# Performance work log

Measured on AMD Instinct MI355X. Metric: run time of the kernel, lower is better.

The kernel has to match this reference:

```python
import jax, jax.numpy as jnp
import numpy as np

G = 5      # kan_grid: number of grid intervals on [-1, 1]
K = 3      # kan_k: B-spline order

def make_grid(in_dim, dtype=jnp.float32):
    # pykan extended grid: uniform on [-1,1] with G intervals, extended by K knots each side
    h = 2.0 / G
    pts = jnp.arange(-K, G + K + 1, dtype=dtype) * h - 1.0   # (G + 2K + 1,)
    return jnp.broadcast_to(pts, (in_dim, G + 2 * K + 1))

def b_spline_basis(x, grid):
    # x: (N, D), grid: (D, M).  Cox-de Boor recursion, vectorized over (N, D).
    xe = x[:, :, None]                      # (N, D, 1)
    g = grid[None, :, :]                    # (1, D, M)
    B = ((xe >= g[:, :, :-1]) & (xe < g[:, :, 1:])).astype(x.dtype)  # order 0
    for p in range(1, K + 1):
        B = ((xe - g[:, :, :-(p + 1)]) / (g[:, :, p:-1] - g[:, :, :-(p + 1)])) * B[:, :, :-1] \
          + ((g[:, :, p + 1:] - xe) / (g[:, :, p + 1:] - g[:, :, 1:-p])) * B[:, :, 1:]
    return B                                # (N, D, G + K)

def kan_layer(x, coef, scale_base, scale_sp):
    # pykan KANLayer: out_o = sum_i [ sb[i,o]*silu(x_i) + ss[i,o]*sum_g B(x_i)_g * coef[i,o,g] ]
    in_dim = x.shape[1]
    B = b_spline_basis(x, make_grid(in_dim, x.dtype))          # (N, D, G+K)
    y_base = jnp.einsum('ni,io->no', jax.nn.silu(x), scale_base)
    y_sp = jnp.einsum('nig,iog,io->no', B, coef, scale_sp)
    return y_base + y_sp

def setup_inputs() -> dict:
    key = jax.random.key(0)
    ks = jax.random.split(key, 5)
    d_model, hidden = 512, 1024
    bsz, seq = 4, 1024
    ncoef = G + K
    x = jax.random.normal(ks[0], (bsz, seq, d_model), dtype=jnp.float32)
    coef1 = 0.1 * jax.random.normal(ks[1], (d_model, hidden, ncoef), dtype=jnp.float32)
    coef2 = 0.1 * jax.random.normal(ks[2], (hidden, d_model, ncoef), dtype=jnp.float32)
    scale_base1 = (1.0 / np.sqrt(d_model)) * jax.random.normal(ks[3], (d_model, hidden), dtype=jnp.float32)
    scale_base2 = (1.0 / np.sqrt(hidden)) * jax.random.normal(ks[4], (hidden, d_model), dtype=jnp.float32)
    scale_sp1 = jnp.ones((d_model, hidden), dtype=jnp.float32)
    scale_sp2 = jnp.ones((hidden, d_model), dtype=jnp.float32)
    return {"x": x, "coef1": coef1, "scale_base1": scale_base1, "scale_sp1": scale_sp1,
            "coef2": coef2, "scale_base2": scale_base2, "scale_sp2": scale_sp2}

def reference(x, coef1, scale_base1, scale_sp1, coef2, scale_base2, scale_sp2):
    bsz, seq, d_model = x.shape
    flat = x.reshape(-1, d_model)                      # (N, d_model); chunking is math-neutral
    h = kan_layer(flat, coef1, scale_base1, scale_sp1)  # (N, hidden)
    out = kan_layer(h, coef2, scale_base2, scale_sp2)   # (N, d_model)
    return out.reshape(bsz, seq, d_model)              # dropout p=0.0 -> identity
```

## Files before the change

kernel.cpp:

```cpp
#include <hip/hip_runtime.h>
#include <hip/hip_bf16.h>
#include <cstdint>
#include <cstddef>

typedef float  f32x4 __attribute__((ext_vector_type(4)));
typedef _Float16 f16x8 __attribute__((ext_vector_type(8)));

#define DEVFN __device__ __forceinline__

DEVFN void bspline8(float x, float bv[8]) {
    float t[12];
#pragma unroll
    for (int j = 0; j < 12; ++j) t[j] = (float)(j - 3) * 0.4f - 1.0f;
    float B[11];
#pragma unroll
    for (int j = 0; j < 11; ++j) B[j] = (x >= t[j] && x < t[j + 1]) ? 1.0f : 0.0f;
    const float rp[3] = {2.5f, 1.25f, 0.8333333333f};
#pragma unroll
    for (int p = 1; p <= 3; ++p) {
#pragma unroll
        for (int j = 0; j + p < 11; ++j) {
            float left  = (x - t[j]) * rp[p - 1];
            float right = (t[j + p + 1] - x) * rp[p - 1];
            B[j] = left * B[j] + right * B[j + 1];
        }
    }
#pragma unroll
    for (int g = 0; g < 8; ++g) bv[g] = B[g];
}

DEVFN void kan_features(float x, _Float16* dst, int D) {
    float s = x * __builtin_amdgcn_rcpf(1.0f + __expf(-x));
    float bv[8];
    bspline8(x, bv);
    dst[0] = (_Float16)s;
#pragma unroll
    for (int g = 0; g < 8; ++g) dst[(size_t)(g + 1) * D] = (_Float16)bv[g];
}

__global__ void prep_a_kernel(const float* __restrict__ X,
                              _Float16* __restrict__ Aaug,
                              int total, int dshift) {
    int idx = blockIdx.x * 256 + threadIdx.x;
    if (idx >= total) return;
    const int D = 1 << dshift;
    const int K = 9 << dshift;
    const int n = idx >> dshift;
    const int i = idx & (D - 1);
    kan_features(X[idx], Aaug + (size_t)n * K + i, D);
}

__global__ void prep_a_red_kernel(const float* __restrict__ HP,
                                  _Float16* __restrict__ Aaug,
                                  int total, int dshift, size_t pstride) {
    int idx = blockIdx.x * 256 + threadIdx.x;
    if (idx >= total) return;
    const int D = 1 << dshift;
    const int K = 9 << dshift;
    const int n = idx >> dshift;
    const int i = idx & (D - 1);
    float x = (HP[idx] + HP[idx + pstride]) +
              (HP[idx + 2 * pstride] + HP[idx + 3 * pstride]);
    kan_features(x, Aaug + (size_t)n * K + i, D);
}

__global__ void reduce_out_kernel(const float* __restrict__ OP,
                                  float* __restrict__ out,
                                  int total4, size_t pstride4) {
    int i = blockIdx.x * 256 + threadIdx.x;
    if (i >= total4) return;
    const f32x4* p = (const f32x4*)OP;
    f32x4 s = p[i];
#pragma unroll
    for (int k = 1; k < 8; ++k) s += p[i + k * pstride4];
    ((f32x4*)out)[i] = s;
}

__global__ void prep_w_kernel(const float* __restrict__ coef,
                              const float* __restrict__ sb,
                              const float* __restrict__ sp,
                              _Float16* __restrict__ WT,
                              int total, int din_shift, int dout) {
    int idx = blockIdx.x * 256 + threadIdx.x;
    if (idx >= total) return;
    const int Din = 1 << din_shift;
    const int i = idx & (Din - 1);
    const int o = idx >> din_shift;
    const size_t K = (size_t)9 << din_shift;
    const size_t cidx = (size_t)i * dout + o;
    float base  = sb[cidx];
    float scale = sp[cidx];
    const float* cp = coef + cidx * 8;
    _Float16* dst = WT + (size_t)o * K + i;
    dst[0] = (_Float16)base;
#pragma unroll
    for (int g = 0; g < 8; ++g) dst[(size_t)(g + 1) * Din] = (_Float16)(cp[g] * scale);
}

DEVFN void gload16(const void* g, void* l) {
    __builtin_amdgcn_global_load_lds(
        (const __attribute__((address_space(1))) void*)g,
        (__attribute__((address_space(3))) void*)l, 16, 0, 0);
}

__global__ __launch_bounds__(512, 2) void gemm256_f16_bt(
    const _Float16* __restrict__ A,
    const _Float16* __restrict__ WT,
    float* __restrict__ P,
    int K, int N, int klen, int gxshift) {
    constexpr int BK = 64;
    __shared__ _Float16 Alds[2][256 * BK];
    __shared__ _Float16 Blds[2][256 * BK];

    const int tid  = threadIdx.x;
    const int lane = tid & 63;
    const int w    = tid >> 6;
    const int wm   = w >> 2;
    const int wn   = w & 3;

    const int gx   = 1 << gxshift;
    const int nwg  = gx * 16 * gridDim.z;
    const int orig = blockIdx.x + (blockIdx.y << gxshift) + blockIdx.z * (gx * 16);
    const int tile = (orig & 7) * (nwg >> 3) + (orig >> 3);
    const int col  = tile & (gx - 1);
    const int rs   = tile >> gxshift;
    const int row  = rs & 15;
    const int spl  = rs >> 4;

    const size_t bm = (size_t)row * 256;
    const size_t bn = (size_t)col * 256;
    const int kbase = spl * klen;
    const int nt    = klen / BK;
    float* Cp = P + (size_t)spl * 4096 * N;

    const f32x4 vzero = {0.0f, 0.0f, 0.0f, 0.0f};
    f32x4 acc[8][4];
#pragma unroll
    for (int m = 0; m < 8; ++m)
#pragma unroll
        for (int n = 0; n < 4; ++n) acc[m][n] = vzero;

    const int srow = tid >> 3;
    const int c8   = tid & 7;
    const int ldst = w * 512;

#define STAGE(b, kk)                                                         \
    {                                                                        \
        _Pragma("unroll")                                                    \
        for (int is = 0; is < 4; ++is) {                                     \
            const int r  = is * 64 + srow;                                   \
            const int sg = (c8 ^ (r & 7)) << 3;                              \
            gload16(A + (bm + r) * (size_t)K + (kk) + sg,                    \
                    &Alds[b][is * 4096 + ldst]);                             \
            gload16(WT + (bn + r) * (size_t)K + (kk) + sg,                   \
                    &Blds[b][is * 4096 + ldst]);                             \
        }                                                                    \
    }

    STAGE(0, kbase);

    for (int t = 0; t < nt; ++t) {
        const int cur = t & 1;
        if (t + 1 < nt) {
            STAGE(cur ^ 1, kbase + (t + 1) * BK);
            asm volatile("s_waitcnt vmcnt(8)" ::: "memory");
        } else {
            asm volatile("s_waitcnt vmcnt(0)" ::: "memory");
        }
        __builtin_amdgcn_s_barrier();
        __builtin_amdgcn_sched_barrier(0);

#pragma unroll
        for (int ks = 0; ks < BK; ks += 32) {
            f16x8 af[8], bf[4];
            const int g = (ks >> 3) + (lane >> 4);
#pragma unroll
            for (int m = 0; m < 8; ++m) {
                const int r2 = wm * 128 + m * 16 + (lane & 15);
                af[m] = *(const f16x8*)(&Alds[cur][r2 * BK + ((g ^ (r2 & 7)) << 3)]);
            }
#pragma unroll
            for (int n = 0; n < 4; ++n) {
                const int r2 = wn * 64 + n * 16 + (lane & 15);
                bf[n] = *(const f16x8*)(&Blds[cur][r2 * BK + ((g ^ (r2 & 7)) << 3)]);
            }
#pragma unroll
            for (int m = 0; m < 8; ++m)
#pragma unroll
                for (int n = 0; n < 4; ++n)
                    acc[m][n] = __builtin_amdgcn_mfma_f32_16x16x32_f16(
                        af[m], bf[n], acc[m][n], 0, 0, 0);
        }
        __builtin_amdgcn_s_barrier();
        __builtin_amdgcn_sched_barrier(0);
    }
#undef STAGE

    const int r0 = wm * 128 + (lane >> 4) * 4;
    const int c0 = wn * 64 + (lane & 15);
#pragma unroll
    for (int m = 0; m < 8; ++m)
#pragma unroll
        for (int n = 0; n < 4; ++n)
#pragma unroll
            for (int r = 0; r < 4; ++r)
                Cp[(bm + r0 + m * 16 + r) * (size_t)N + bn + c0 + n * 16] =
                    acc[m][n][r];
}

extern "C" void kernel_launch(void* const* d_in, const int* in_sizes, int n_in,
                              void* d_out, int out_size, void* d_ws, size_t ws_size,
                              hipStream_t stream) {
    const float* x     = (const float*)d_in[0];
    const float* coef1 = (const float*)d_in[1];
    const float* sb1   = (const float*)d_in[2];
    const float* sp1   = (const float*)d_in[3];
    const float* coef2 = (const float*)d_in[4];
    const float* sb2   = (const float*)d_in[5];
    const float* sp2   = (const float*)d_in[6];
    float* out = (float*)d_out;

    const int M  = 4096;
    const int D1 = 512;
    const int D2 = 1024;
    const int K1 = 9 * D1;
    const int K2 = 9 * D2;

    char* ws = (char*)d_ws;
    _Float16* Aaug = (_Float16*)ws;
    _Float16* WT   = (_Float16*)(ws + (size_t)M * K2 * 2);
    float*    P    = (float*)(ws + (size_t)M * K2 * 2 +
                              (size_t)D1 * K2 * 2);

    prep_w_kernel<<<(D1 * D2) / 256, 256, 0, stream>>>(coef1, sb1, sp1, WT,
                                                       D1 * D2, 9, D2);
    prep_a_kernel<<<(M * D1) / 256, 256, 0, stream>>>(x, Aaug, M * D1, 9);
    {
        dim3 grid(D2 / 256, M / 256, 4);
        gemm256_f16_bt<<<grid, 512, 0, stream>>>(Aaug, WT, P, K1, D2, K1 / 4, 2);
    }
    prep_w_kernel<<<(D2 * D1) / 256, 256, 0, stream>>>(coef2, sb2, sp2, WT,
                                                       D1 * D2, 10, D1);
    prep_a_red_kernel<<<(M * D2) / 256, 256, 0, stream>>>(P, Aaug, M * D2, 10,
                                                          (size_t)M * D2);
    {
        dim3 grid(D1 / 256, M / 256, 8);
        gemm256_f16_bt<<<grid, 512, 0, stream>>>(Aaug, WT, P, K2, D1, K2 / 8, 1);
    }
    reduce_out_kernel<<<(M * D1 / 4) / 256, 256, 0, stream>>>(
        P, out, M * D1 / 4, (size_t)M * D1 / 4);
}
```

Measured before the change: 252.6 us.

## Split GEMM inner loop into quadrant phases with setprio and vectorize feature prep

The GEMM main loop now runs in four quadrant phases. Each phase loads only part of the A/B fragments from LDS and issues its MFMAs between s_setprio raises and barriers, so LDS reads interleave with matrix math across waves and register pressure drops. The A-feature prep kernels now handle four elements per thread with vector loads and f16x4 stores, cutting the number of narrow global accesses. The extra barriers per tile could add synchronization stalls.

```diff
diff --git a/kernel.cpp b/kernel.cpp
--- a/kernel.cpp
+++ b/kernel.cpp
@@ -5,6 +5,7 @@
 
 typedef float  f32x4 __attribute__((ext_vector_type(4)));
 typedef _Float16 f16x8 __attribute__((ext_vector_type(8)));
+typedef _Float16 f16x4 __attribute__((ext_vector_type(4)));
 
 #define DEVFN __device__ __forceinline__
 
@@ -29,39 +30,69 @@
     for (int g = 0; g < 8; ++g) bv[g] = B[g];
 }
 
-DEVFN void kan_features(float x, _Float16* dst, int D) {
-    float s = x * __builtin_amdgcn_rcpf(1.0f + __expf(-x));
-    float bv[8];
-    bspline8(x, bv);
-    dst[0] = (_Float16)s;
-#pragma unroll
-    for (int g = 0; g < 8; ++g) dst[(size_t)(g + 1) * D] = (_Float16)bv[g];
+DEVFN float silu_f(float x) {
+    return x * __builtin_amdgcn_rcpf(1.0f + __expf(-x));
 }
 
 __global__ void prep_a_kernel(const float* __restrict__ X,
                               _Float16* __restrict__ Aaug,
-                              int total, int dshift) {
+                              int total4, int dshift) {
     int idx = blockIdx.x * 256 + threadIdx.x;
-    if (idx >= total) return;
-    const int D = 1 << dshift;
-    const int K = 9 << dshift;
-    const int n = idx >> dshift;
-    const int i = idx & (D - 1);
-    kan_features(X[idx], Aaug + (size_t)n * K + i, D);
+    if (idx >= total4) return;
+    const int D  = 1 << dshift;
+    const int K  = 9 << dshift;
+    const int dq = dshift - 2;
+    const int n  = idx >> dq;
+    const int i4 = (idx & ((1 << dq) - 1)) << 2;
+    f32x4 x = *(const f32x4*)(X + (size_t)n * D + i4);
+    float bv[4][8];
+    f16x4 v;
+#pragma unroll
+    for (int e = 0; e < 4; ++e) {
+        v[e] = (_Float16)silu_f(x[e]);
+        bspline8(x[e], bv[e]);
+    }
+    _Float16* dst = Aaug + (size_t)n * K + i4;
+    *(f16x4*)dst = v;
+#pragma unroll
+    for (int g = 0; g < 8; ++g) {
+        f16x4 u;
+#pragma unroll
+        for (int e = 0; e < 4; ++e) u[e] = (_Float16)bv[e][g];
+        *(f16x4*)(dst + (size_t)(g + 1) * D) = u;
+    }
 }
 
 __global__ void prep_a_red_kernel(const float* __restrict__ HP,
                                   _Float16* __restrict__ Aaug,
-                                  int total, int dshift, size_t pstride) {
+                                  int total4, int dshift, size_t pstride) {
     int idx = blockIdx.x * 256 + threadIdx.x;
-    if (idx >= total) return;
-    const int D = 1 << dshift;
-    const int K = 9 << dshift;
-    const int n = idx >> dshift;
-    const int i = idx & (D - 1);
-    float x = (HP[idx] + HP[idx + pstride]) +
-              (HP[idx + 2 * pstride] + HP[idx + 3 * pstride]);
-    kan_features(x, Aaug + (size_t)n * K + i, D);
+    if (idx >= total4) return;
+    const int D  = 1 << dshift;
+    const int K  = 9 << dshift;
+    const int dq = dshift - 2;
+    const int n  = idx >> dq;
+    const int i4 = (idx & ((1 << dq) - 1)) << 2;
+    const size_t off = (size_t)n * D + i4;
+    f32x4 x = (*(const f32x4*)(HP + off) + *(const f32x4*)(HP + off + pstride)) +
+              (*(const f32x4*)(HP + off + 2 * pstride) +
+               *(const f32x4*)(HP + off + 3 * pstride));
+    float bv[4][8];
+    f16x4 v;
+#pragma unroll
+    for (int e = 0; e < 4; ++e) {
+        v[e] = (_Float16)silu_f(x[e]);
+        bspline8(x[e], bv[e]);
+    }
+    _Float16* dst = Aaug + (size_t)n * K + i4;
+    *(f16x4*)dst = v;
+#pragma unroll
+    for (int g = 0; g < 8; ++g) {
+        f16x4 u;
+#pragma unroll
+        for (int e = 0; e < 4; ++e) u[e] = (_Float16)bv[e][g];
+        *(f16x4*)(dst + (size_t)(g + 1) * D) = u;
+    }
 }
 
 __global__ void reduce_out_kernel(const float* __restrict__ OP,
@@ -143,6 +174,8 @@
     const int srow = tid >> 3;
     const int c8   = tid & 7;
     const int ldst = w * 512;
+    const int l15  = lane & 15;
+    const int gk   = lane >> 4;
 
 #define STAGE(b, kk)                                                         \
     {                                                                        \
@@ -157,6 +190,11 @@
         }                                                                    \
     }
 
+#define AADDR(buf, r2, ks2) \
+    (&Alds[buf][(r2) * BK + (((((ks2) * 4) + gk) ^ ((r2) & 7)) << 3)])
+#define BADDR(buf, r2, ks2) \
+    (&Blds[buf][(r2) * BK + (((((ks2) * 4) + gk) ^ ((r2) & 7)) << 3)])
+
     STAGE(0, kbase);
 
     for (int t = 0; t < nt; ++t) {
@@ -170,31 +208,91 @@
         __builtin_amdgcn_s_barrier();
         __builtin_amdgcn_sched_barrier(0);
 
-#pragma unroll
-        for (int ks = 0; ks < BK; ks += 32) {
-            f16x8 af[8], bf[4];
-            const int g = (ks >> 3) + (lane >> 4);
-#pragma unroll
-            for (int m = 0; m < 8; ++m) {
-                const int r2 = wm * 128 + m * 16 + (lane & 15);
-                af[m] = *(const f16x8*)(&Alds[cur][r2 * BK + ((g ^ (r2 & 7)) << 3)]);
+        f16x8 af[4][2], bf0[2][2], bf1[2][2];
+
+#pragma unroll
+        for (int m = 0; m < 4; ++m)
+#pragma unroll
+            for (int ks = 0; ks < 2; ++ks) {
+                const int r2 = wm * 128 + m * 16 + l15;
+                af[m][ks] = *(const f16x8*)AADDR(cur, r2, ks);
             }
 #pragma unroll
-            for (int n = 0; n < 4; ++n) {
-                const int r2 = wn * 64 + n * 16 + (lane & 15);
-                bf[n] = *(const f16x8*)(&Blds[cur][r2 * BK + ((g ^ (r2 & 7)) << 3)]);
+        for (int n = 0; n < 2; ++n)
+#pragma unroll
+            for (int ks = 0; ks < 2; ++ks) {
+                const int r2 = wn * 64 + n * 16 + l15;
+                bf0[n][ks] = *(const f16x8*)BADDR(cur, r2, ks);
             }
-#pragma unroll
-            for (int m = 0; m < 8; ++m)
-#pragma unroll
-                for (int n = 0; n < 4; ++n)
+        __builtin_amdgcn_s_setprio(1);
+#pragma unroll
+        for (int m = 0; m < 4; ++m)
+#pragma unroll
+            for (int n = 0; n < 2; ++n)
+#pragma unroll
+                for (int ks = 0; ks < 2; ++ks)
                     acc[m][n] = __builtin_amdgcn_mfma_f32_16x16x32_f16(
-                        af[m], bf[n], acc[m][n], 0, 0, 0);
-        }
+                        af[m][ks], bf0[n][ks], acc[m][n], 0, 0, 0);
+        __builtin_amdgcn_s_setprio(0);
+        __builtin_amdgcn_s_barrier();
+        __builtin_amdgcn_sched_barrier(0);
+
+#pragma unroll
+        for (int n = 0; n < 2; ++n)
+#pragma unroll
+            for (int ks = 0; ks < 2; ++ks) {
+                const int r2 = wn * 64 + 32 + n * 16 + l15;
+                bf1[n][ks] = *(const f16x8*)BADDR(cur, r2, ks);
+            }
+        __builtin_amdgcn_s_setprio(1);
+#pragma unroll
+        for (int m = 0; m < 4; ++m)
+#pragma unroll
+            for (int n = 0; n < 2; ++n)
+#pragma unroll
+                for (int ks = 0; ks < 2; ++ks)
+                    acc[m][n + 2] = __builtin_amdgcn_mfma_f32_16x16x32_f16(
+                        af[m][ks], bf1[n][ks], acc[m][n + 2], 0, 0, 0);
+        __builtin_amdgcn_s_setprio(0);
+        __builtin_amdgcn_s_barrier();
+        __builtin_amdgcn_sched_barrier(0);
+
+#pragma unroll
+        for (int m = 0; m < 4; ++m)
+#pragma unroll
+            for (int ks = 0; ks < 2; ++ks) {
+                const int r2 = wm * 128 + 64 + m * 16 + l15;
+                af[m][ks] = *(const f16x8*)AADDR(cur, r2, ks);
+            }
+        __builtin_amdgcn_s_setprio(1);
+#pragma unroll
+        for (int m = 0; m < 4; ++m)
+#pragma unroll
+            for (int n = 0; n < 2; ++n)
+#pragma unroll
+                for (int ks = 0; ks < 2; ++ks)
+                    acc[m + 4][n + 2] = __builtin_amdgcn_mfma_f32_16x16x32_f16(
+                        af[m][ks], bf1[n][ks], acc[m + 4][n + 2], 0, 0, 0);
+        __builtin_amdgcn_s_setprio(0);
+        __builtin_amdgcn_s_barrier();
+        __builtin_amdgcn_sched_barrier(0);
+
+        __builtin_amdgcn_s_setprio(1);
+#pragma unroll
+        for (int m = 0; m < 4; ++m)
+#pragma unroll
+            for (int n = 0; n < 2; ++n)
+#pragma unroll
+                for (int ks = 0; ks < 2; ++ks)
+                    acc[m + 4][n] = __builtin_amdgcn_mfma_f32_16x16x32_f16(
+                        af[m][ks], bf0[n][ks], acc[m + 4][n], 0, 0, 0);
+        __builtin_amdgcn_s_setprio(0);
         __builtin_amdgcn_s_barrier();
         __builtin_amdgcn_sched_barrier(0);
     }
 #undef STAGE
+#undef AADDR
+#undef BADDR
 
     const int r0 = wm * 128 + (lane >> 4) * 4;
     const int c0 = wn * 64 + (lane & 15);
@@ -234,15 +332,15 @@
 
     prep_w_kernel<<<(D1 * D2) / 256, 256, 0, stream>>>(coef1, sb1, sp1, WT,
                                                        D1 * D2, 9, D2);
-    prep_a_kernel<<<(M * D1) / 256, 256, 0, stream>>>(x, Aaug, M * D1, 9);
+    prep_a_kernel<<<(M * D1 / 4) / 256, 256, 0, stream>>>(x, Aaug, M * D1 / 4, 9);
     {
         dim3 grid(D2 / 256, M / 256, 4);
         gemm256_f16_bt<<<grid, 512, 0, stream>>>(Aaug, WT, P, K1, D2, K1 / 4, 2);
     }
     prep_w_kernel<<<(D2 * D1) / 256, 256, 0, stream>>>(coef2, sb2, sp2, WT,
                                                        D1 * D2, 10, D1);
-    prep_a_red_kernel<<<(M * D2) / 256, 256, 0, stream>>>(P, Aaug, M * D2, 10,
-                                                          (size_t)M * D2);
+    prep_a_red_kernel<<<(M * D2 / 4) / 256, 256, 0, stream>>>(
+        P, Aaug, M * D2 / 4, 10, (size_t)M * D2);
     {
         dim3 grid(D1 / 256, M / 256, 8);
         gemm256_f16_bt<<<grid, 512, 0, stream>>>(Aaug, WT, P, K2, D1, K2 / 8, 1);
```

Measured after the change: 257.1 us. No clear change (+1.8%).
